# Performance work log

Measured on AMD Instinct MI355X. Metric: run time of the kernel, lower is better.

## Reference

```python
import jax, jax.numpy as jnp
import numpy as np

D_MODEL = 1024
N_HEADS = 16
HEAD_DIM = D_MODEL // N_HEADS
NEG_INF = -1e9


def setup_inputs() -> dict:
    key = jax.random.key(0)
    ks = jax.random.split(key, 6)
    B, T, C = 4, 2048, D_MODEL
    x = jax.random.normal(ks[0], (B, T, C), dtype=jnp.float32)
    # causal mask, broadcastable over batch and heads
    mask = jnp.tril(jnp.ones((T, T), dtype=jnp.int32))[None, None]
    scale = 1.0 / np.sqrt(C)
    W_qkv = jax.random.normal(ks[1], (3 * C, C), dtype=jnp.float32) * scale
    b_qkv = jnp.zeros((3 * C,), dtype=jnp.float32)
    W_out = jax.random.normal(ks[2], (C, C), dtype=jnp.float32) * scale
    b_out = jnp.zeros((C,), dtype=jnp.float32)
    return {"x": x, "mask": mask, "W_qkv": W_qkv, "b_qkv": b_qkv,
            "W_out": W_out, "b_out": b_out}


def reference(x, mask, W_qkv, b_qkv, W_out, b_out):
    B, T, C = x.shape
    H, D = N_HEADS, HEAD_DIM
    qkv = x @ W_qkv.T + b_qkv                      # [B, T, 3C]
    q, k, v = jnp.split(qkv, 3, axis=-1)
    # [B, T, C] -> [B, H, T, D]
    q = q.reshape(B, T, H, D).transpose(0, 2, 1, 3)
    k = k.reshape(B, T, H, D).transpose(0, 2, 1, 3)
    v = v.reshape(B, T, H, D).transpose(0, 2, 1, 3)
    scores = jnp.einsum("bhqd,bhkd->bhqk", q, k) / np.sqrt(D)
    scores = jnp.where(mask == 0, NEG_INF, scores)
    att = jax.nn.softmax(scores, axis=-1)          # dropout p=0 (eval)
    out = jnp.einsum("bhqk,bhkd->bhqd", att, v)    # [B, H, T, D]
    out = out.transpose(0, 2, 1, 3).reshape(B, T, C)
    return out @ W_out.T + b_out
```

## Files before the change

kernel.cpp:

```cpp
#include <hip/hip_runtime.h>
#include <hip/hip_bf16.h>

typedef unsigned short u16;
typedef unsigned int u32;
using short8 = __attribute__((ext_vector_type(8))) short;
using f32x4  = __attribute__((ext_vector_type(4))) float;
using f32x16 = __attribute__((ext_vector_type(16))) float;
using uint2v = __attribute__((ext_vector_type(2))) u32;

#define T_SEQ 2048
#define C_DIM 1024
#define NH 16
#define HD 64

#if __has_builtin(__builtin_amdgcn_exp2f)
#define EXP2(x) __builtin_amdgcn_exp2f(x)
#else
#define EXP2(x) exp2f(x)
#endif

__device__ __forceinline__ u16 f2bf(float f) {
    unsigned int u = __float_as_uint(f);
    unsigned int r = (u + 0x7fffu + ((u >> 16) & 1u)) >> 16;
    return (u16)r;
}
__device__ __forceinline__ u32 cvtpk(float lo, float hi) {
    u32 r;
    asm("v_cvt_pk_bf16_f32 %0, %1, %2" : "=v"(r) : "v"(lo), "v"(hi));
    return r;
}
__device__ __forceinline__ short8 mk8(u32 a, u32 b, u32 c, u32 d) {
    union { u32 u[4]; short8 s; } t;
    t.u[0] = a; t.u[1] = b; t.u[2] = c; t.u[3] = d;
    return t.s;
}
__device__ __forceinline__ void gl_lds16(const u16* g, u16* l) {
    __builtin_amdgcn_global_load_lds(
        (const __attribute__((address_space(1))) unsigned int*)g,
        (__attribute__((address_space(3))) unsigned int*)l, 16, 0, 0);
}
template <int N> __device__ __forceinline__ void s_vmcnt();
template <> __device__ __forceinline__ void s_vmcnt<0>() {
    asm volatile("s_waitcnt vmcnt(0)" ::: "memory");
}
template <> __device__ __forceinline__ void s_vmcnt<2>() {
    asm volatile("s_waitcnt vmcnt(2)" ::: "memory");
}
template <> __device__ __forceinline__ void s_vmcnt<4>() {
    asm volatile("s_waitcnt vmcnt(4)" ::: "memory");
}
template <> __device__ __forceinline__ void s_vmcnt<8>() {
    asm volatile("s_waitcnt vmcnt(8)" ::: "memory");
}
__device__ __forceinline__ void BAR() {
    asm volatile("" ::: "memory");
    __builtin_amdgcn_s_barrier();
    asm volatile("" ::: "memory");
}

__global__ __launch_bounds__(256) void cvt_all(const float* __restrict__ x,
                                               u16* __restrict__ ox, int n0,
                                               const float* __restrict__ a,
                                               u16* __restrict__ oa, int n1,
                                               const float* __restrict__ b,
                                               u16* __restrict__ ob, int n2) {
    int i = blockIdx.x * blockDim.x + threadIdx.x;
    const float* src;
    u16* dst;
    if (i < n0) { src = x; dst = ox; }
    else if (i < n0 + n1) { src = a; dst = oa; i -= n0; }
    else if (i < n0 + n1 + n2) { src = b; dst = ob; i -= n0 + n1; }
    else return;
    const float4* p = (const float4*)src + (size_t)i * 2;
    float4 u = p[0], v = p[1];
    short8 o;
    o[0] = (short)f2bf(u.x); o[1] = (short)f2bf(u.y);
    o[2] = (short)f2bf(u.z); o[3] = (short)f2bf(u.w);
    o[4] = (short)f2bf(v.x); o[5] = (short)f2bf(v.y);
    o[6] = (short)f2bf(v.z); o[7] = (short)f2bf(v.w);
    *(short8*)(dst + (size_t)i * 8) = o;
}

template <int EPI, int NX>
__global__ __launch_bounds__(256) void gemm_bt(const u16* __restrict__ A,
                                               const u16* __restrict__ Bt,
                                               const float* __restrict__ bias,
                                               u16* __restrict__ qb, u16* __restrict__ kb,
                                               u16* __restrict__ vtb, float* __restrict__ Cf,
                                               int M, int N, int K) {
    __shared__ __align__(16) u16 Al[3][128][32];
    __shared__ __align__(16) u16 Bl[3][128][32];
    const int tid = threadIdx.x;
    const int lane = tid & 63, wid = tid >> 6;
    const int li = lane & 15, g = lane >> 4;
    const int wr = (wid >> 1) * 64, wc = (wid & 1) * 64;

    const int bid = blockIdx.x;
    const int xcd = bid & 7;
    const int r_ = bid >> 3;
    const int xq = r_ >> 5;
    const int rem = r_ & 31;
    const int yloc = rem >> 2, xr = rem & 3;
    const size_t m0 = (size_t)(xcd * 8 + yloc) * 128;
    const size_t n0 = (size_t)(xq * 4 + xr) * 128;

    const int srow = lane >> 2;
    const int sch = (lane & 3) ^ ((srow >> 1) & 3);
    const u16* aA = A + (m0 + wid * 32 + srow) * (size_t)K + sch * 8;
    const u16* aB = Bt + (n0 + wid * 32 + srow) * (size_t)K + sch * 8;

    f32x4 acc[4][4] = {};
    const int nt = K / 32;

    auto STAGE = [&](int buf, int k0) {
        gl_lds16(aA + k0, &Al[buf][wid * 32][0]);
        gl_lds16(aA + 16 * (size_t)K + k0, &Al[buf][wid * 32 + 16][0]);
        gl_lds16(aB + k0, &Bl[buf][wid * 32][0]);
        gl_lds16(aB + 16 * (size_t)K + k0, &Bl[buf][wid * 32 + 16][0]);
    };

    STAGE(0, 0);
    STAGE(1, 32);
    int cur = 0;
#pragma unroll 1
    for (int t = 0; t < nt; ++t) {
        if (t + 2 < nt) {
            int bs = cur + 2; if (bs >= 3) bs -= 3;
            STAGE(bs, (t + 2) * 32);
            s_vmcnt<8>();
        } else if (t + 1 < nt) {
            s_vmcnt<4>();
        } else {
            s_vmcnt<0>();
        }
        BAR();
        short8 af[4], bf[4];
#pragma unroll
        for (int i = 0; i < 4; i++) {
            int row = wr + i * 16 + li;
            af[i] = *(const short8*)&Al[cur][row][(g ^ ((row >> 1) & 3)) * 8];
        }
#pragma unroll
        for (int i = 0; i < 4; i++) {
            int row = wc + i * 16 + li;
            bf[i] = *(const short8*)&Bl[cur][row][(g ^ ((row >> 1) & 3)) * 8];
        }
        __builtin_amdgcn_s_setprio(1);
#pragma unroll
        for (int mi = 0; mi < 4; mi++)
#pragma unroll
            for (int ni = 0; ni < 4; ni++)
                acc[mi][ni] = __builtin_amdgcn_mfma_f32_16x16x32_bf16(af[mi], bf[ni],
                                                                      acc[mi][ni], 0, 0, 0);
        __builtin_amdgcn_s_setprio(0);
        BAR();
        cur = (cur == 2) ? 0 : cur + 1;
    }

#pragma unroll
    for (int mi = 0; mi < 4; mi++)
#pragma unroll
        for (int ni = 0; ni < 4; ni++) {
            size_t col = n0 + wc + ni * 16 + li;
            size_t row0 = m0 + wr + mi * 16 + g * 4;
            if (EPI == 0) {
                int which = (int)(col >> 10);
                int rem2 = (int)(col & 1023);
                int h = rem2 >> 6, d = rem2 & 63;
                size_t b = row0 >> 11, t0v = row0 & 2047;
                float bv = bias[col];
                if (which == 2) {
                    ushort4 o4;
                    o4.x = f2bf(acc[mi][ni][0] + bv);
                    o4.y = f2bf(acc[mi][ni][1] + bv);
                    o4.z = f2bf(acc[mi][ni][2] + bv);
                    o4.w = f2bf(acc[mi][ni][3] + bv);
                    *(ushort4*)(vtb + (((b * NH) + h) * (size_t)HD + d) * T_SEQ + t0v) = o4;
                } else {
                    u16* dst = (which == 0) ? qb : kb;
                    float sc = (which == 0) ? 0.18033688f : 1.0f;
#pragma unroll
                    for (int r = 0; r < 4; r++)
                        dst[(((b * NH) + h) * T_SEQ + t0v + r) * HD + d] =
                            f2bf((acc[mi][ni][r] + bv) * sc);
                }
            } else {
                float bv = bias[col];
#pragma unroll
                for (int r = 0; r < 4; r++)
                    Cf[(row0 + r) * (size_t)N + col] = acc[mi][ni][r] + bv;
            }
        }
}

__global__ __launch_bounds__(512) void attn_fwd2(const u16* __restrict__ Q,
                                                 const u16* __restrict__ K,
                                                 const u16* __restrict__ Vt,
                                                 u16* __restrict__ O) {
    __shared__ __align__(16) u16 KL[2][64 * 64];
    __shared__ __align__(16) u16 VL[2][64 * 64];
    const int tid = threadIdx.x;
    const int lane = tid & 63, wid = tid >> 6;
    const int l31 = lane & 31, hi = lane >> 5;

    const int wg = blockIdx.x;
    const int j = wg >> 8, c = wg & 255;
    const int xcd = c & 7, m = c >> 3;
    const int bh = (xcd << 3) | (m >> 2);
    const int v = m & 3;
    const int qt = j ? v : (7 - v);

    const size_t bhT = (size_t)bh * T_SEQ;
    const int srow8 = lane >> 3, sch = (lane & 7) ^ srow8;
    const int b = bh >> 4, h = bh & 15;
    const int x7 = l31 & 7;

    const int q0 = qt * 256;
    const int qw0 = q0 + wid * 32;
    const int nkt = 4 * qt + 4;

    short8 qf[4];
    {
        const u16* qp = Q + (bhT + qw0 + l31) * HD + hi * 8;
#pragma unroll
        for (int s = 0; s < 4; s++) qf[s] = *(const short8*)(qp + s * 16);
    }

    f32x16 o0 = {}, o1 = {};
    float l_run = 0.f;

    gl_lds16(K + (bhT + wid * 8 + srow8) * HD + sch * 8, &KL[0][wid * 8 * 64]);
    gl_lds16(Vt + ((size_t)bh * HD + wid * 8 + srow8) * T_SEQ + sch * 8,
             &VL[0][wid * 8 * 64]);

    for (int kt = 0; kt < nkt; kt++) {
        if (kt + 1 < nkt) {
            const int kv0n = (kt + 1) * 64;
            const int nb = (kt + 1) & 1;
            gl_lds16(K + (bhT + kv0n + wid * 8 + srow8) * HD + sch * 8,
                     &KL[nb][wid * 8 * 64]);
            gl_lds16(Vt + ((size_t)bh * HD + wid * 8 + srow8) * T_SEQ + kv0n + sch * 8,
                     &VL[nb][wid * 8 * 64]);
            s_vmcnt<2>();
        } else {
            s_vmcnt<0>();
        }
        BAR();

        const int kv0 = kt * 64;
        if (kv0 <= qw0) {
            const u16* KLb = KL[kt & 1];
            const u16* VLb = VL[kt & 1];

            f32x16 s0 = {}, s1 = {};
            __builtin_amdgcn_s_setprio(1);
#pragma unroll
            for (int sl = 0; sl < 4; sl++) {
                int ch = ((sl * 2 + hi) ^ x7) * 8;
                short8 ka = *(const short8*)&KLb[l31 * 64 + ch];
                s0 = __builtin_amdgcn_mfma_f32_32x32x16_bf16(ka, qf[sl], s0, 0, 0, 0);
                short8 kb2 = *(const short8*)&KLb[(32 + l31) * 64 + ch];
                s1 = __builtin_amdgcn_mfma_f32_32x32x16_bf16(kb2, qf[sl], s1, 0, 0, 0);
            }
            __builtin_amdgcn_s_setprio(0);

            const int qg = qw0 + l31;
            if (kv0 + 63 > qw0) {
#pragma unroll
                for (int r = 0; r < 16; r++) {
                    int kvr = kv0 + (r & 3) + 8 * (r >> 2) + 4 * hi;
                    if (kvr > qg) s0[r] = -1e30f;
                    if (kvr + 32 > qg) s1[r] = -1e30f;
                }
            }

            float ls = 0.f;
#pragma unroll
            for (int r = 0; r < 16; r++) {
                float p = EXP2(s0[r]);
                s0[r] = p; ls += p;
            }
            {
                u32 c0 = cvtpk(s0[0], s0[1]),   c1 = cvtpk(s0[2], s0[3]),
                    c2 = cvtpk(s0[4], s0[5]),   c3 = cvtpk(s0[6], s0[7]),
                    c4 = cvtpk(s0[8], s0[9]),   c5 = cvtpk(s0[10], s0[11]),
                    c6 = cvtpk(s0[12], s0[13]), c7 = cvtpk(s0[14], s0[15]);
                uint2v wA = __builtin_amdgcn_permlane32_swap(c0, c2, false, false);
                uint2v wB = __builtin_amdgcn_permlane32_swap(c1, c3, false, false);
                uint2v wC = __builtin_amdgcn_permlane32_swap(c4, c6, false, false);
                uint2v wD = __builtin_amdgcn_permlane32_swap(c5, c7, false, false);
                short8 paA = mk8(wA[0], wB[0], wA[1], wB[1]);
                short8 paB = mk8(wC[0], wD[0], wC[1], wD[1]);
                __builtin_amdgcn_s_setprio(1);
#pragma unroll
                for (int sl = 0; sl < 2; sl++) {
                    short8 pa = (sl == 0) ? paA : paB;
                    int ch = ((sl * 2 + hi) ^ x7) * 8;
                    short8 va = *(const short8*)&VLb[l31 * 64 + ch];
                    o0 = __builtin_amdgcn_mfma_f32_32x32x16_bf16(pa, va, o0, 0, 0, 0);
                    short8 vb2 = *(const short8*)&VLb[(32 + l31) * 64 + ch];
                    o1 = __builtin_amdgcn_mfma_f32_32x32x16_bf16(pa, vb2, o1, 0, 0, 0);
                }
                __builtin_amdgcn_s_setprio(0);
            }
#pragma unroll
            for (int r = 0; r < 16; r++) {
                float p = EXP2(s1[r]);
                s1[r] = p; ls += p;
            }
            {
                u32 c0 = cvtpk(s1[0], s1[1]),   c1 = cvtpk(s1[2], s1[3]),
                    c2 = cvtpk(s1[4], s1[5]),   c3 = cvtpk(s1[6], s1[7]),
                    c4 = cvtpk(s1[8], s1[9]),   c5 = cvtpk(s1[10], s1[11]),
                    c6 = cvtpk(s1[12], s1[13]), c7 = cvtpk(s1[14], s1[15]);
                uint2v wA = __builtin_amdgcn_permlane32_swap(c0, c2, false, false);
                uint2v wB = __builtin_amdgcn_permlane32_swap(c1, c3, false, false);
                uint2v wC = __builtin_amdgcn_permlane32_swap(c4, c6, false, false);
                uint2v wD = __builtin_amdgcn_permlane32_swap(c5, c7, false, false);
                short8 paC = mk8(wA[0], wB[0], wA[1], wB[1]);
                short8 paD = mk8(wC[0], wD[0], wC[1], wD[1]);
                __builtin_amdgcn_s_setprio(1);
#pragma unroll
                for (int sl = 2; sl < 4; sl++) {
                    short8 pa = (sl == 2) ? paC : paD;
                    int ch = ((sl * 2 + hi) ^ x7) * 8;
                    short8 va = *(const short8*)&VLb[l31 * 64 + ch];
                    o0 = __builtin_amdgcn_mfma_f32_32x32x16_bf16(pa, va, o0, 0, 0, 0);
                    short8 vb2 = *(const short8*)&VLb[(32 + l31) * 64 + ch];
                    o1 = __builtin_amdgcn_mfma_f32_32x32x16_bf16(pa, vb2, o1, 0, 0, 0);
                }
                __builtin_amdgcn_s_setprio(0);
            }
            ls += __shfl_xor(ls, 32);
            l_run += ls;
        }
        BAR();
    }

    const float inv = 1.0f / l_run;
#pragma unroll
    for (int r = 0; r < 16; r++) {
        int qr = (r & 3) + 8 * (r >> 2) + 4 * hi;
        float invr = __shfl(inv, qr);
        int t = q0 + wid * 32 + qr;
        size_t rowoff = ((size_t)b * T_SEQ + t) * C_DIM + h * HD;
        O[rowoff + l31]      = f2bf(o0[r] * invr);
        O[rowoff + 32 + l31] = f2bf(o1[r] * invr);
    }
}

extern "C" void kernel_launch(void* const* d_in, const int* in_sizes, int n_in,
                              void* d_out, int out_size, void* d_ws, size_t ws_size,
                              hipStream_t stream) {
    const float* x     = (const float*)d_in[0];
    const float* W_qkv = (const float*)d_in[2];
    const float* b_qkv = (const float*)d_in[3];
    const float* W_out = (const float*)d_in[4];
    const float* b_out = (const float*)d_in[5];
    float* out = (float*)d_out;

    char* w = (char*)d_ws;
    u16* xb    = (u16*)(w);
    u16* wqkvb = (u16*)(w + 16777216);
    u16* woutb = (u16*)(w + 23068672);
    u16* qb    = (u16*)(w + 25165824);
    u16* kb    = (u16*)(w + 41943040);
    u16* vtb   = (u16*)(w + 58720256);
    u16* attnb = xb;

    cvt_all<<<6144, 256, 0, stream>>>(x, xb, 1048576, W_qkv, wqkvb, 393216,
                                      W_out, woutb, 131072);

    gemm_bt<0, 24><<<1536, 256, 0, stream>>>(xb, wqkvb, b_qkv, qb, kb, vtb, nullptr,
                                             8192, 3072, 1024);

    attn_fwd2<<<512, 512, 0, stream>>>(qb, kb, vtb, attnb);

    gemm_bt<1, 8><<<512, 256, 0, stream>>>(attnb, woutb, b_out, nullptr, nullptr,
                                           nullptr, out, 8192, 1024, 1024);
}
```

Before: 158.6 us.

## Software-pipeline PV matmul with next QK tile using triple-buffered V

The attention kernel now uses 256-thread blocks covering 128 query rows and launches 1024 blocks, with a four-way q-tile assignment meant to balance causal work. The P·V MFMAs for tile kt are deferred and issued after the QK^T MFMAs of tile kt+1, so matrix work overlaps the softmax exponentials. V gets a third LDS buffer so the deferred PV can still read its tile while the next loads land. This adds register pressure from holding P fragments across iterations and changes the occupancy and scheduling balance.

Measured after the change: 173.5 us. 1.09x slower.

```diff
diff --git a/kernel.cpp b/kernel.cpp
--- a/kernel.cpp
+++ b/kernel.cpp
@@ -42,9 +42,6 @@
 template <int N> __device__ __forceinline__ void s_vmcnt();
 template <> __device__ __forceinline__ void s_vmcnt<0>() {
     asm volatile("s_waitcnt vmcnt(0)" ::: "memory");
-}
-template <> __device__ __forceinline__ void s_vmcnt<2>() {
-    asm volatile("s_waitcnt vmcnt(2)" ::: "memory");
 }
 template <> __device__ __forceinline__ void s_vmcnt<4>() {
     asm volatile("s_waitcnt vmcnt(4)" ::: "memory");
@@ -193,12 +190,12 @@
         }
 }
 
-__global__ __launch_bounds__(512) void attn_fwd2(const u16* __restrict__ Q,
+__global__ __launch_bounds__(256) void attn_fwd2(const u16* __restrict__ Q,
                                                  const u16* __restrict__ K,
                                                  const u16* __restrict__ Vt,
                                                  u16* __restrict__ O) {
     __shared__ __align__(16) u16 KL[2][64 * 64];
-    __shared__ __align__(16) u16 VL[2][64 * 64];
+    __shared__ __align__(16) u16 VL[3][64 * 64];
     const int tid = threadIdx.x;
     const int lane = tid & 63, wid = tid >> 6;
     const int l31 = lane & 31, hi = lane >> 5;
@@ -208,16 +205,16 @@
     const int xcd = c & 7, m = c >> 3;
     const int bh = (xcd << 3) | (m >> 2);
     const int v = m & 3;
-    const int qt = j ? v : (7 - v);
+    const int qt = (j == 0) ? (15 - v) : (j == 1) ? v : (j == 2) ? (11 - v) : (v + 4);
 
     const size_t bhT = (size_t)bh * T_SEQ;
-    const int srow8 = lane >> 3, sch = (lane & 7) ^ srow8;
+    const int srow8 = lane >> 3, sch = lane & 7;
     const int b = bh >> 4, h = bh & 15;
     const int x7 = l31 & 7;
 
-    const int q0 = qt * 256;
+    const int q0 = qt * 128;
     const int qw0 = q0 + wid * 32;
-    const int nkt = 4 * qt + 4;
+    const int nkt = 2 * qt + 2;
 
     short8 qf[4];
     {
@@ -228,20 +225,50 @@
 
     f32x16 o0 = {}, o1 = {};
     float l_run = 0.f;
-
-    gl_lds16(K + (bhT + wid * 8 + srow8) * HD + sch * 8, &KL[0][wid * 8 * 64]);
-    gl_lds16(Vt + ((size_t)bh * HD + wid * 8 + srow8) * T_SEQ + sch * 8,
-             &VL[0][wid * 8 * 64]);
+    short8 pA = {}, pB = {}, pC = {}, pD = {};
+    int vprev = 0;
+    bool pend = false;
+
+    auto PV = [&](int vp) {
+        const u16* VLb = VL[vp];
+        __builtin_amdgcn_s_setprio(1);
+#pragma unroll
+        for (int sl = 0; sl < 4; sl++) {
+            short8 pa = (sl == 0) ? pA : (sl == 1) ? pB : (sl == 2) ? pC : pD;
+            int ch = ((sl * 2 + hi) ^ x7) * 8;
+            short8 va = *(const short8*)&VLb[l31 * 64 + ch];
+            o0 = __builtin_amdgcn_mfma_f32_32x32x16_bf16(pa, va, o0, 0, 0, 0);
+            short8 vb2 = *(const short8*)&VLb[(32 + l31) * 64 + ch];
+            o1 = __builtin_amdgcn_mfma_f32_32x32x16_bf16(pa, vb2, o1, 0, 0, 0);
+        }
+        __builtin_amdgcn_s_setprio(0);
+    };
+
+#pragma unroll
+    for (int i = 0; i < 2; i++) {
+        int row = wid * 16 + i * 8 + srow8;
+        int ch = sch ^ (row & 7);
+        gl_lds16(K + (bhT + row) * HD + ch * 8, &KL[0][(wid * 16 + i * 8) * 64]);
+        gl_lds16(Vt + ((size_t)bh * HD + row) * T_SEQ + ch * 8,
+                 &VL[0][(wid * 16 + i * 8) * 64]);
+    }
 
     for (int kt = 0; kt < nkt; kt++) {
         if (kt + 1 < nkt) {
             const int kv0n = (kt + 1) * 64;
-            const int nb = (kt + 1) & 1;
-            gl_lds16(K + (bhT + kv0n + wid * 8 + srow8) * HD + sch * 8,
-                     &KL[nb][wid * 8 * 64]);
-            gl_lds16(Vt + ((size_t)bh * HD + wid * 8 + srow8) * T_SEQ + kv0n + sch * 8,
-                     &VL[nb][wid * 8 * 64]);
-            s_vmcnt<2>();
+            const int kb2i = (kt + 1) & 1;
+            int vb3 = kt + 1; vb3 -= (vb3 >= 3) ? 3 : 0; vb3 -= (vb3 >= 3) ? 3 : 0;
+            int vbuf = (kt + 1) % 3;
+#pragma unroll
+            for (int i = 0; i < 2; i++) {
+                int row = wid * 16 + i * 8 + srow8;
+                int ch = sch ^ (row & 7);
+                gl_lds16(K + (bhT + kv0n + row) * HD + ch * 8,
+                         &KL[kb2i][(wid * 16 + i * 8) * 64]);
+                gl_lds16(Vt + ((size_t)bh * HD + row) * T_SEQ + kv0n + ch * 8,
+                         &VL[vbuf][(wid * 16 + i * 8) * 64]);
+            }
+            s_vmcnt<4>();
         } else {
             s_vmcnt<0>();
         }
@@ -250,7 +277,6 @@
         const int kv0 = kt * 64;
         if (kv0 <= qw0) {
             const u16* KLb = KL[kt & 1];
-            const u16* VLb = VL[kt & 1];
 
             f32x16 s0 = {}, s1 = {};
             __builtin_amdgcn_s_setprio(1);
@@ -263,6 +289,7 @@
                 s1 = __builtin_amdgcn_mfma_f32_32x32x16_bf16(kb2, qf[sl], s1, 0, 0, 0);
             }
             __builtin_amdgcn_s_setprio(0);
+            if (pend) PV(vprev);
 
             const int qg = qw0 + l31;
             if (kv0 + 63 > qw0) {
@@ -277,9 +304,13 @@
             float ls = 0.f;
 #pragma unroll
             for (int r = 0; r < 16; r++) {
-                float p = EXP2(s0[r]);
-                s0[r] = p; ls += p;
-            }
+                float p0 = EXP2(s0[r]);
+                float p1 = EXP2(s1[r]);
+                s0[r] = p0; s1[r] = p1;
+                ls += p0 + p1;
+            }
+            ls += __shfl_xor(ls, 32);
+            l_run += ls;
             {
                 u32 c0 = cvtpk(s0[0], s0[1]),   c1 = cvtpk(s0[2], s0[3]),
                     c2 = cvtpk(s0[4], s0[5]),   c3 = cvtpk(s0[6], s0[7]),
@@ -289,24 +320,8 @@
                 uint2v wB = __builtin_amdgcn_permlane32_swap(c1, c3, false, false);
                 uint2v wC = __builtin_amdgcn_permlane32_swap(c4, c6, false, false);
                 uint2v wD = __builtin_amdgcn_permlane32_swap(c5, c7, false, false);
-                short8 paA = mk8(wA[0], wB[0], wA[1], wB[1]);
-                short8 paB = mk8(wC[0], wD[0], wC[1], wD[1]);
-                __builtin_amdgcn_s_setprio(1);
-#pragma unroll
-                for (int sl = 0; sl < 2; sl++) {
-                    short8 pa = (sl == 0) ? paA : paB;
-                    int ch = ((sl * 2 + hi) ^ x7) * 8;
-                    short8 va = *(const short8*)&VLb[l31 * 64 + ch];
-                    o0 = __builtin_amdgcn_mfma_f32_32x32x16_bf16(pa, va, o0, 0, 0, 0);
-                    short8 vb2 = *(const short8*)&VLb[(32 + l31) * 64 + ch];
-                    o1 = __builtin_amdgcn_mfma_f32_32x32x16_bf16(pa, vb2, o1, 0, 0, 0);
-                }
-                __builtin_amdgcn_s_setprio(0);
-            }
-#pragma unroll
-            for (int r = 0; r < 16; r++) {
-                float p = EXP2(s1[r]);
-                s1[r] = p; ls += p;
+                pA = mk8(wA[0], wB[0], wA[1], wB[1]);
+                pB = mk8(wC[0], wD[0], wC[1], wD[1]);
             }
             {
                 u32 c0 = cvtpk(s1[0], s1[1]),   c1 = cvtpk(s1[2], s1[3]),
@@ -317,25 +332,18 @@
                 uint2v wB = __builtin_amdgcn_permlane32_swap(c1, c3, false, false);
                 uint2v wC = __builtin_amdgcn_permlane32_swap(c4, c6, false, false);
                 uint2v wD = __builtin_amdgcn_permlane32_swap(c5, c7, false, false);
-                short8 paC = mk8(wA[0], wB[0], wA[1], wB[1]);
-                short8 paD = mk8(wC[0], wD[0], wC[1], wD[1]);
-                __builtin_amdgcn_s_setprio(1);
-#pragma unroll
-                for (int sl = 2; sl < 4; sl++) {
-                    short8 pa = (sl == 2) ? paC : paD;
-                    int ch = ((sl * 2 + hi) ^ x7) * 8;
-                    short8 va = *(const short8*)&VLb[l31 * 64 + ch];
-                    o0 = __builtin_amdgcn_mfma_f32_32x32x16_bf16(pa, va, o0, 0, 0, 0);
-                    short8 vb2 = *(const short8*)&VLb[(32 + l31) * 64 + ch];
-                    o1 = __builtin_amdgcn_mfma_f32_32x32x16_bf16(pa, vb2, o1, 0, 0, 0);
-                }
-                __builtin_amdgcn_s_setprio(0);
-            }
-            ls += __shfl_xor(ls, 32);
-            l_run += ls;
+                pC = mk8(wA[0], wB[0], wA[1], wB[1]);
+                pD = mk8(wC[0], wD[0], wC[1], wD[1]);
+            }
+            vprev = kt % 3;
+            pend = true;
+        } else if (pend) {
+            PV(vprev);
+            pend = false;
         }
         BAR();
     }
+    if (pend) PV(vprev);
 
     const float inv = 1.0f / l_run;
 #pragma unroll
@@ -374,7 +382,7 @@
     gemm_bt<0, 24><<<1536, 256, 0, stream>>>(xb, wqkvb, b_qkv, qb, kb, vtb, nullptr,
                                              8192, 3072, 1024);
 
-    attn_fwd2<<<512, 512, 0, stream>>>(qb, kb, vtb, attnb);
+    attn_fwd2<<<1024, 256, 0, stream>>>(qb, kb, vtb, attnb);
 
     gemm_bt<1, 8><<<512, 256, 0, stream>>>(attnb, woutb, b_out, nullptr, nullptr,
                                            nullptr, out, 8192, 1024, 1024);
```
